# Performance work log

Hardware: AMD Instinct MI355X
Metric: run time of the kernel (lower is better)

The kernel has to match this reference:

```python
import jax, jax.numpy as jnp
import numpy as np

N_NODES = 50000
N_EDGES = 800000
IN_CH, HIDDEN, OUT_CH = 128, 128, 64
EPS = 1e-5


def setup_inputs() -> dict:
    key = jax.random.key(0)
    ks = jax.random.split(key, 16)
    s = lambda fan_in: 1.0 / np.sqrt(fan_in)
    return {
        "x": jax.random.normal(ks[0], (N_NODES, IN_CH), dtype=jnp.float32),
        "edge_index": jax.random.randint(ks[1], (2, N_EDGES), 0, N_NODES, dtype=jnp.int64),
        # SAGEConv1: lin_l (neighbors, with bias), lin_r (root, no bias)
        "Wl1": jax.random.uniform(ks[2], (HIDDEN, IN_CH), jnp.float32, -s(IN_CH), s(IN_CH)),
        "bl1": jnp.zeros((HIDDEN,), jnp.float32),
        "Wr1": jax.random.uniform(ks[3], (HIDDEN, IN_CH), jnp.float32, -s(IN_CH), s(IN_CH)),
        # SAGEConv2
        "Wl2": jax.random.uniform(ks[4], (HIDDEN, HIDDEN), jnp.float32, -s(HIDDEN), s(HIDDEN)),
        "bl2": jnp.zeros((HIDDEN,), jnp.float32),
        "Wr2": jax.random.uniform(ks[5], (HIDDEN, HIDDEN), jnp.float32, -s(HIDDEN), s(HIDDEN)),
        # SAGEConv3
        "Wl3": jax.random.uniform(ks[6], (OUT_CH, HIDDEN), jnp.float32, -s(HIDDEN), s(HIDDEN)),
        "bl3": jnp.zeros((OUT_CH,), jnp.float32),
        "Wr3": jax.random.uniform(ks[7], (OUT_CH, HIDDEN), jnp.float32, -s(HIDDEN), s(HIDDEN)),
        # LayerNorms
        "g1": jnp.ones((HIDDEN,), jnp.float32),
        "beta1": jnp.zeros((HIDDEN,), jnp.float32),
        "g2": jnp.ones((HIDDEN,), jnp.float32),
        "beta2": jnp.zeros((HIDDEN,), jnp.float32),
    }


def _sage_conv(x, src, dst, n_nodes, Wl, bl, Wr):
    # mean aggregation of source features at target nodes (PyG SAGEConv, aggr='mean')
    msg = x[src]                                             # [E, C] gather
    sums = jax.ops.segment_sum(msg, dst, num_segments=n_nodes)
    cnt = jax.ops.segment_sum(jnp.ones((src.shape[0],), x.dtype), dst, num_segments=n_nodes)
    mean = sums / jnp.maximum(cnt, 1.0)[:, None]
    return mean @ Wl.T + bl + x @ Wr.T


def _layernorm(h, g, b):
    mu = jnp.mean(h, axis=-1, keepdims=True)
    var = jnp.mean(jnp.square(h - mu), axis=-1, keepdims=True)
    return (h - mu) * jax.lax.rsqrt(var + EPS) * g + b


def reference(x, edge_index, Wl1, bl1, Wr1, Wl2, bl2, Wr2, Wl3, bl3, Wr3, g1, beta1, g2, beta2):
    src, dst = edge_index[0], edge_index[1]
    n = x.shape[0]
    h = jax.nn.relu(_sage_conv(x, src, dst, n, Wl1, bl1, Wr1))
    h = _layernorm(h, g1, beta1)
    h = jax.nn.relu(_sage_conv(h, src, dst, n, Wl2, bl2, Wr2))
    h = _layernorm(h, g2, beta2)
    return _sage_conv(h, src, dst, n, Wl3, bl3, Wr3)
```

## Files before the change

kernel.cpp:

```cpp
#include <hip/hip_runtime.h>

#define NNODES 50000
#define NEDGES 800000
#define FILL_CHUNK 7168
#define FILL_NCHUNK 112
#define FILL_BLOCKS (FILL_NCHUNK * 8)
#define GEMM_BLOCKS ((NNODES + 127) / 128)
#define CAP 64

using bf16x8  = __attribute__((ext_vector_type(8))) __bf16;
using floatx4 = __attribute__((ext_vector_type(4))) float;

__device__ __forceinline__ float bf2f(unsigned short u) {
  unsigned int v = ((unsigned int)u) << 16;
  return __builtin_bit_cast(float, v);
}
__device__ __forceinline__ unsigned short f2bf(float f) {
  unsigned int u = __builtin_bit_cast(unsigned int, f);
  u += 0x7fffu + ((u >> 16) & 1u);
  return (unsigned short)(u >> 16);
}

__device__ __forceinline__ signed char enc_i8(float f) {
  float g = fminf(fmaxf(f * 32.0f, -127.0f), 127.0f);
  return (signed char)__float2int_rn(g);
}

struct WPtrs {
  const float* src[6];
  unsigned short* dst[6];
  int n[6];
};

__global__ __launch_bounds__(256) void convw_zero_kernel(WPtrs p, int* __restrict__ cnt) {
  if (blockIdx.x < 320) {
    int i = blockIdx.x * 256 + threadIdx.x;
#pragma unroll
    for (int s = 0; s < 6; ++s) {
      if (i < p.n[s]) {
        p.dst[s][i] = f2bf(p.src[s][i]);
        return;
      }
      i -= p.n[s];
    }
  } else {
    int i = (blockIdx.x - 320) * 256 + threadIdx.x;
    if (i < NNODES) cnt[i] = 0;
  }
}

__device__ __forceinline__ void fill_body(int bid, const int* __restrict__ src,
                                          const int* __restrict__ dst,
                                          int* __restrict__ cnt,
                                          int* __restrict__ bucket) {
  int p = bid & 7;
  if (p == 7) return;
  int chunk = bid >> 3;
  int e0 = chunk * FILL_CHUNK;
  int e1 = min(e0 + FILL_CHUNK, NEDGES);
  for (int base = e0 + (int)threadIdx.x * 4; base < e1; base += 256 * 4) {
    int4 d4 = *(const int4*)(dst + base);
    int4 s4 = *(const int4*)(src + base);
    if ((d4.x >> 13) == p) { int sl = atomicAdd(&cnt[d4.x], 1); if (sl < CAP) bucket[(size_t)d4.x * CAP + sl] = s4.x; }
    if ((d4.y >> 13) == p) { int sl = atomicAdd(&cnt[d4.y], 1); if (sl < CAP) bucket[(size_t)d4.y * CAP + sl] = s4.y; }
    if ((d4.z >> 13) == p) { int sl = atomicAdd(&cnt[d4.z], 1); if (sl < CAP) bucket[(size_t)d4.z * CAP + sl] = s4.z; }
    if ((d4.w >> 13) == p) { int sl = atomicAdd(&cnt[d4.w], 1); if (sl < CAP) bucket[(size_t)d4.w * CAP + sl] = s4.w; }
  }
}

__device__ __forceinline__ bf16x8 load_frag(const unsigned short* p) {
  uint4 v = *(const uint4*)p;
  return __builtin_bit_cast(bf16x8, v);
}
__device__ __forceinline__ bf16x8 cvt_frag(const float* p) {
  float4 v0 = *(const float4*)p;
  float4 v1 = *(const float4*)(p + 4);
  uint4 o;
  o.x = (unsigned int)f2bf(v0.x) | ((unsigned int)f2bf(v0.y) << 16);
  o.y = (unsigned int)f2bf(v0.z) | ((unsigned int)f2bf(v0.w) << 16);
  o.z = (unsigned int)f2bf(v1.x) | ((unsigned int)f2bf(v1.y) << 16);
  o.w = (unsigned int)f2bf(v1.z) | ((unsigned int)f2bf(v1.w) << 16);
  return __builtin_bit_cast(bf16x8, o);
}

template <int NTL, int NTR, bool F32IN>
__device__ __forceinline__ void gemm_dual_body(int bid, const void* __restrict__ Ain,
                                               const unsigned short* __restrict__ W,
                                               signed char* __restrict__ yl,
                                               unsigned short* __restrict__ yr) {
  constexpr int NT = NTL + NTR;
  int wave = threadIdx.x >> 6;
  int lane = threadIdx.x & 63;
  int quad = lane >> 4;
  int m = lane & 15;
  int row0 = bid * 128 + wave * 32;
  int ar0 = min(row0 + m, NNODES - 1);
  int ar1 = min(row0 + 16 + m, NNODES - 1);
  bf16x8 a0[4], a1[4];
#pragma unroll
  for (int kt = 0; kt < 4; ++kt) {
    if constexpr (F32IN) {
      const float* A = (const float*)Ain;
      a0[kt] = cvt_frag(A + (size_t)ar0 * 128 + quad * 8 + kt * 32);
      a1[kt] = cvt_frag(A + (size_t)ar1 * 128 + quad * 8 + kt * 32);
    } else {
      const unsigned short* A = (const unsigned short*)Ain;
      a0[kt] = load_frag(A + (size_t)ar0 * 128 + quad * 8 + kt * 32);
      a1[kt] = load_frag(A + (size_t)ar1 * 128 + quad * 8 + kt * 32);
    }
  }
#pragma unroll
  for (int t = 0; t < NT; ++t) {
    const unsigned short* wp = W + (t * 16 + m) * 128 + quad * 8;
    bf16x8 w[4];
#pragma unroll
    for (int kt = 0; kt < 4; ++kt) w[kt] = load_frag(wp + kt * 32);
    floatx4 c0 = {0.f, 0.f, 0.f, 0.f};
    floatx4 c1 = {0.f, 0.f, 0.f, 0.f};
#pragma unroll
    for (int kt = 0; kt < 4; ++kt) {
      c0 = __builtin_amdgcn_mfma_f32_16x16x32_bf16(a0[kt], w[kt], c0, 0, 0, 0);
      c1 = __builtin_amdgcn_mfma_f32_16x16x32_bf16(a1[kt], w[kt], c1, 0, 0, 0);
    }
#pragma unroll
    for (int r = 0; r < 4; ++r) {
      int g0 = row0 + quad * 4 + r;
      int g1r = g0 + 16;
      if (t < NTL) {
        int col = t * 16 + m;
        if (g0 < NNODES) yl[(size_t)g0 * (NTL * 16) + col] = enc_i8(c0[r]);
        if (g1r < NNODES) yl[(size_t)g1r * (NTL * 16) + col] = enc_i8(c1[r]);
      } else {
        int col = (t - NTL) * 16 + m;
        if (g0 < NNODES) yr[(size_t)g0 * (NTR * 16) + col] = f2bf(c0[r]);
        if (g1r < NNODES) yr[(size_t)g1r * (NTR * 16) + col] = f2bf(c1[r]);
      }
    }
  }
}

__global__ __launch_bounds__(256) void fill_gemm1_kernel(
    const int* __restrict__ src, const int* __restrict__ dst, int* __restrict__ cnt,
    int* __restrict__ bucket, const float* __restrict__ x,
    const unsigned short* __restrict__ W, signed char* __restrict__ yl,
    unsigned short* __restrict__ yr) {
  if (blockIdx.x < FILL_BLOCKS)
    fill_body(blockIdx.x, src, dst, cnt, bucket);
  else
    gemm_dual_body<8, 8, true>(blockIdx.x - FILL_BLOCKS, x, W, yl, yr);
}

template <int NTL, int NTR, bool F32IN>
__global__ __launch_bounds__(256) void gemm_dual_kernel(
    const void* __restrict__ Ain, const unsigned short* __restrict__ W,
    signed char* __restrict__ yl, unsigned short* __restrict__ yr) {
  gemm_dual_body<NTL, NTR, F32IN>(blockIdx.x, Ain, W, yl, yr);
}

#define ACCU(u, base)                                       \
  a[base] += (int)((signed char)((u) & 0xffu));             \
  a[base + 1] += (int)((signed char)(((u) >> 8) & 0xffu));  \
  a[base + 2] += (int)((signed char)(((u) >> 16) & 0xffu)); \
  a[base + 3] += (int)((signed char)((u) >> 24));
#define ACC16(v) ACCU((v).x, 0) ACCU((v).y, 4) ACCU((v).z, 8) ACCU((v).w, 12)

__global__ __launch_bounds__(256) void agg_ln_kernel(
    const signed char* __restrict__ yl, const unsigned short* __restrict__ yr,
    const float* __restrict__ bl, const float* __restrict__ g,
    const float* __restrict__ be, const int* __restrict__ cnt,
    const int* __restrict__ bucket, unsigned short* __restrict__ hout) {
  int wid = (blockIdx.x * blockDim.x + threadIdx.x) >> 6;
  int lane = threadIdx.x & 63;
  int grp = lane >> 3;
  int c8 = lane & 7;
  int gw = wid * 8 + grp;
  if (gw >= NNODES) return;
  int offc = c8 * 16;
  int deg = cnt[gw];
  int ed = min(deg, CAP);
  const int* bk = bucket + (size_t)gw * CAP;
  int a[16];
#pragma unroll
  for (int k = 0; k < 16; ++k) a[k] = 0;
  int e = 0;
  for (; e + 3 < ed; e += 4) {
    int i0 = bk[e], i1 = bk[e + 1], i2 = bk[e + 2], i3 = bk[e + 3];
    uint4 v0 = *(const uint4*)(yl + (size_t)i0 * 128 + offc);
    uint4 v1 = *(const uint4*)(yl + (size_t)i1 * 128 + offc);
    uint4 v2 = *(const uint4*)(yl + (size_t)i2 * 128 + offc);
    uint4 v3 = *(const uint4*)(yl + (size_t)i3 * 128 + offc);
    ACC16(v0) ACC16(v1) ACC16(v2) ACC16(v3)
  }
  if (e + 1 < ed) {
    int i0 = bk[e], i1 = bk[e + 1];
    uint4 v0 = *(const uint4*)(yl + (size_t)i0 * 128 + offc);
    uint4 v1 = *(const uint4*)(yl + (size_t)i1 * 128 + offc);
    ACC16(v0) ACC16(v1)
    e += 2;
  }
  if (e < ed) {
    int i0 = bk[e];
    uint4 v = *(const uint4*)(yl + (size_t)i0 * 128 + offc);
    ACC16(v)
  }
  float idg = 0.03125f / (float)((deg > 0) ? deg : 1);
  const unsigned short* yrp = yr + (size_t)gw * 128 + offc;
  uint4 r0 = *(const uint4*)yrp;
  uint4 r1 = *(const uint4*)(yrp + 8);
  unsigned rw[8] = {r0.x, r0.y, r0.z, r0.w, r1.x, r1.y, r1.z, r1.w};
  float blv[16], gv[16], bev[16];
#pragma unroll
  for (int k = 0; k < 4; ++k) {
    *(float4*)&blv[k * 4] = *(const float4*)(bl + offc + k * 4);
    *(float4*)&gv[k * 4] = *(const float4*)(g + offc + k * 4);
    *(float4*)&bev[k * 4] = *(const float4*)(be + offc + k * 4);
  }
  float x[16], sA = 0.f, sB = 0.f;
#pragma unroll
  for (int k = 0; k < 16; ++k) {
    float rv = bf2f((unsigned short)((rw[k >> 1] >> ((k & 1) * 16)) & 0xffffu));
    float xv = (float)a[k] * idg + rv + blv[k];
    xv = fmaxf(xv, 0.f);
    x[k] = xv;
    sA += xv;
    sB += xv * xv;
  }
#pragma unroll
  for (int msk = 1; msk < 8; msk <<= 1) {
    sA += __shfl_xor(sA, msk, 8);
    sB += __shfl_xor(sB, msk, 8);
  }
  float mu = sA * (1.0f / 128.0f);
  float var = sB * (1.0f / 128.0f) - mu * mu;
  float rs = rsqrtf(var + 1e-5f);
  unsigned ow[8];
#pragma unroll
  for (int k = 0; k < 8; ++k) {
    float y0 = (x[2 * k] - mu) * rs * gv[2 * k] + bev[2 * k];
    float y1 = (x[2 * k + 1] - mu) * rs * gv[2 * k + 1] + bev[2 * k + 1];
    ow[k] = (unsigned)f2bf(y0) | ((unsigned)f2bf(y1) << 16);
  }
  uint4* op = (uint4*)(hout + (size_t)gw * 128 + offc);
  op[0] = make_uint4(ow[0], ow[1], ow[2], ow[3]);
  op[1] = make_uint4(ow[4], ow[5], ow[6], ow[7]);
}

__global__ __launch_bounds__(256) void agg3_kernel(
    const signed char* __restrict__ yl, const unsigned short* __restrict__ yr,
    const float* __restrict__ bl, const int* __restrict__ cnt,
    const int* __restrict__ bucket, float* __restrict__ out) {
  int wid = (blockIdx.x * blockDim.x + threadIdx.x) >> 6;
  int lane = threadIdx.x & 63;
  int grp = lane >> 2;
  int c4 = lane & 3;
  int gw = wid * 16 + grp;
  if (gw >= NNODES) return;
  int offc = c4 * 16;
  int deg = cnt[gw];
  int ed = min(deg, CAP);
  const int* bk = bucket + (size_t)gw * CAP;
  int a[16];
#pragma unroll
  for (int k = 0; k < 16; ++k) a[k] = 0;
  int e = 0;
  for (; e + 3 < ed; e += 4) {
    int i0 = bk[e], i1 = bk[e + 1], i2 = bk[e + 2], i3 = bk[e + 3];
    uint4 v0 = *(const uint4*)(yl + (size_t)i0 * 64 + offc);
    uint4 v1 = *(const uint4*)(yl + (size_t)i1 * 64 + offc);
    uint4 v2 = *(const uint4*)(yl + (size_t)i2 * 64 + offc);
    uint4 v3 = *(const uint4*)(yl + (size_t)i3 * 64 + offc);
    ACC16(v0) ACC16(v1) ACC16(v2) ACC16(v3)
  }
  if (e + 1 < ed) {
    int i0 = bk[e], i1 = bk[e + 1];
    uint4 v0 = *(const uint4*)(yl + (size_t)i0 * 64 + offc);
    uint4 v1 = *(const uint4*)(yl + (size_t)i1 * 64 + offc);
    ACC16(v0) ACC16(v1)
    e += 2;
  }
  if (e < ed) {
    int i0 = bk[e];
    uint4 v = *(const uint4*)(yl + (size_t)i0 * 64 + offc);
    ACC16(v)
  }
  float idg = 0.03125f / (float)((deg > 0) ? deg : 1);
  const unsigned short* yrp = yr + (size_t)gw * 64 + offc;
  uint4 r0 = *(const uint4*)yrp;
  uint4 r1 = *(const uint4*)(yrp + 8);
  unsigned rw[8] = {r0.x, r0.y, r0.z, r0.w, r1.x, r1.y, r1.z, r1.w};
  float blv[16];
#pragma unroll
  for (int k = 0; k < 4; ++k)
    *(float4*)&blv[k * 4] = *(const float4*)(bl + offc + k * 4);
  float o[16];
#pragma unroll
  for (int k = 0; k < 16; ++k) {
    float rv = bf2f((unsigned short)((rw[k >> 1] >> ((k & 1) * 16)) & 0xffffu));
    o[k] = (float)a[k] * idg + rv + blv[k];
  }
  float* op = out + (size_t)gw * 64 + offc;
#pragma unroll
  for (int k = 0; k < 4; ++k) *(float4*)(op + k * 4) = *(float4*)&o[k * 4];
}

extern "C" void kernel_launch(void* const* d_in, const int* in_sizes, int n_in,
                              void* d_out, int out_size, void* d_ws, size_t ws_size,
                              hipStream_t stream) {
  const float* x = (const float*)d_in[0];
  const int* ei = (const int*)d_in[1];
  const int* srcv = ei;
  const int* dstv = ei + NEDGES;
  const float* Wl1 = (const float*)d_in[2];
  const float* bl1 = (const float*)d_in[3];
  const float* Wr1 = (const float*)d_in[4];
  const float* Wl2 = (const float*)d_in[5];
  const float* bl2 = (const float*)d_in[6];
  const float* Wr2 = (const float*)d_in[7];
  const float* Wl3 = (const float*)d_in[8];
  const float* bl3 = (const float*)d_in[9];
  const float* Wr3 = (const float*)d_in[10];
  const float* g1 = (const float*)d_in[11];
  const float* be1 = (const float*)d_in[12];
  const float* g2 = (const float*)d_in[13];
  const float* be2 = (const float*)d_in[14];

  char* ws = (char*)d_ws;
  size_t o = 0;
  int* cnt = (int*)(ws + o);      o += 200192;
  int* bucket = (int*)(ws + o);   o += (size_t)NNODES * CAP * 4;
  unsigned short* wb1 = (unsigned short*)(ws + o); o += 65536;
  unsigned short* wb2 = (unsigned short*)(ws + o); o += 65536;
  unsigned short* wb3 = (unsigned short*)(ws + o); o += 32768;
  signed char* yl1 = (signed char*)(ws + o);       o += (size_t)50000 * 128;
  unsigned short* yr1 = (unsigned short*)(ws + o); o += (size_t)50000 * 256;
  unsigned short* h1 = (unsigned short*)(ws + o);  o += (size_t)50000 * 256;
  signed char* yl2 = (signed char*)(ws + o);       o += (size_t)50000 * 128;
  unsigned short* yr2 = (unsigned short*)(ws + o); o += (size_t)50000 * 256;
  unsigned short* h2 = (unsigned short*)(ws + o);  o += (size_t)50000 * 256;
  signed char* yl3 = (signed char*)(ws + o);       o += (size_t)50000 * 64;
  unsigned short* yr3 = (unsigned short*)(ws + o); o += (size_t)50000 * 128;

  dim3 blk(256);
  dim3 aggGrid((NNODES + 31) / 32);
  dim3 agg3Grid((NNODES + 63) / 64);
  dim3 gemmGrid(GEMM_BLOCKS);

  WPtrs wp;
  wp.src[0] = Wl1; wp.dst[0] = wb1;         wp.n[0] = 128 * 128;
  wp.src[1] = Wr1; wp.dst[1] = wb1 + 16384; wp.n[1] = 128 * 128;
  wp.src[2] = Wl2; wp.dst[2] = wb2;         wp.n[2] = 128 * 128;
  wp.src[3] = Wr2; wp.dst[3] = wb2 + 16384; wp.n[3] = 128 * 128;
  wp.src[4] = Wl3; wp.dst[4] = wb3;         wp.n[4] = 64 * 128;
  wp.src[5] = Wr3; wp.dst[5] = wb3 + 8192;  wp.n[5] = 64 * 128;

  convw_zero_kernel<<<dim3(320 + 196), blk, 0, stream>>>(wp, cnt);
  fill_gemm1_kernel<<<dim3(FILL_BLOCKS + GEMM_BLOCKS), blk, 0, stream>>>(
      srcv, dstv, cnt, bucket, x, wb1, yl1, yr1);
  agg_ln_kernel<<<aggGrid, blk, 0, stream>>>(yl1, yr1, bl1, g1, be1, cnt, bucket, h1);
  gemm_dual_kernel<8, 8, false><<<gemmGrid, blk, 0, stream>>>(h1, wb2, yl2, yr2);
  agg_ln_kernel<<<aggGrid, blk, 0, stream>>>(yl2, yr2, bl2, g2, be2, cnt, bucket, h2);
  gemm_dual_kernel<4, 4, false><<<gemmGrid, blk, 0, stream>>>(h2, wb3, yl3, yr3);
  agg3_kernel<<<agg3Grid, blk, 0, stream>>>(yl3, yr3, bl3, cnt, bucket, (float*)d_out);
}
```

Baseline: 242.5 us.

## Queue fill edges in LDS and pad degree counters to avoid atomic contention

The bucket-fill phase now compacts matching edges into a shared-memory queue with wave ballots, then issues global atomics and nontemporal bucket stores in a separate batched phase. Degree counters are strided (32 or 4 ints apart, depending on workspace size) so that atomics to neighbouring nodes land on different cache lines. Edge loads are also made nontemporal. The aim is to cut atomic contention and memory-latency stalls in the fill, at the cost of a larger counter array to zero, strided counter reads in the aggregation kernels, and a queue capped at QCAP entries that could drop edges if a block's partition overflows it.

```diff
diff --git a/kernel.cpp b/kernel.cpp
--- a/kernel.cpp
+++ b/kernel.cpp
@@ -7,9 +7,11 @@
 #define FILL_BLOCKS (FILL_NCHUNK * 8)
 #define GEMM_BLOCKS ((NNODES + 127) / 128)
 #define CAP 64
+#define QCAP 2048
 
 using bf16x8  = __attribute__((ext_vector_type(8))) __bf16;
 using floatx4 = __attribute__((ext_vector_type(4))) float;
+using intx4   = __attribute__((ext_vector_type(4))) int;
 
 __device__ __forceinline__ float bf2f(unsigned short u) {
   unsigned int v = ((unsigned int)u) << 16;
@@ -32,7 +34,8 @@
   int n[6];
 };
 
-__global__ __launch_bounds__(256) void convw_zero_kernel(WPtrs p, int* __restrict__ cnt) {
+__global__ __launch_bounds__(256) void convw_zero_kernel(WPtrs p, int* __restrict__ cnt,
+                                                         int tot4) {
   if (blockIdx.x < 320) {
     int i = blockIdx.x * 256 + threadIdx.x;
 #pragma unroll
@@ -45,26 +48,69 @@
     }
   } else {
     int i = (blockIdx.x - 320) * 256 + threadIdx.x;
-    if (i < NNODES) cnt[i] = 0;
+    int4* q = (int4*)cnt;
+    int j0 = i * 2, j1 = i * 2 + 1;
+    int4 z = make_int4(0, 0, 0, 0);
+    if (j0 < tot4) q[j0] = z;
+    if (j1 < tot4) q[j1] = z;
   }
 }
 
 __device__ __forceinline__ void fill_body(int bid, const int* __restrict__ src,
                                           const int* __restrict__ dst,
                                           int* __restrict__ cnt,
-                                          int* __restrict__ bucket) {
+                                          int* __restrict__ bucket, int cs) {
   int p = bid & 7;
   if (p == 7) return;
+  __shared__ int qd[QCAP];
+  __shared__ int qs[QCAP];
+  __shared__ int qn;
+  if (threadIdx.x == 0) qn = 0;
+  __syncthreads();
+  int lane = threadIdx.x & 63;
   int chunk = bid >> 3;
   int e0 = chunk * FILL_CHUNK;
   int e1 = min(e0 + FILL_CHUNK, NEDGES);
   for (int base = e0 + (int)threadIdx.x * 4; base < e1; base += 256 * 4) {
-    int4 d4 = *(const int4*)(dst + base);
-    int4 s4 = *(const int4*)(src + base);
-    if ((d4.x >> 13) == p) { int sl = atomicAdd(&cnt[d4.x], 1); if (sl < CAP) bucket[(size_t)d4.x * CAP + sl] = s4.x; }
-    if ((d4.y >> 13) == p) { int sl = atomicAdd(&cnt[d4.y], 1); if (sl < CAP) bucket[(size_t)d4.y * CAP + sl] = s4.y; }
-    if ((d4.z >> 13) == p) { int sl = atomicAdd(&cnt[d4.z], 1); if (sl < CAP) bucket[(size_t)d4.z * CAP + sl] = s4.z; }
-    if ((d4.w >> 13) == p) { int sl = atomicAdd(&cnt[d4.w], 1); if (sl < CAP) bucket[(size_t)d4.w * CAP + sl] = s4.w; }
+    intx4 d4 = __builtin_nontemporal_load((const intx4*)(dst + base));
+    intx4 s4 = __builtin_nontemporal_load((const intx4*)(src + base));
+    int dv[4] = {d4[0], d4[1], d4[2], d4[3]};
+    int sv[4] = {s4[0], s4[1], s4[2], s4[3]};
+#pragma unroll
+    for (int k = 0; k < 4; ++k) {
+      bool mk = (dv[k] >> 13) == p;
+      unsigned long long mask = __ballot(mk);
+      if (mask) {
+        int ldr = __builtin_ctzll(mask);
+        int basq = 0;
+        if (lane == ldr) basq = atomicAdd(&qn, (int)__popcll(mask));
+        basq = __shfl(basq, ldr);
+        if (mk) {
+          int t = basq + (int)__popcll(mask & ((1ull << lane) - 1ull));
+          if (t < QCAP) { qd[t] = dv[k]; qs[t] = sv[k]; }
+        }
+      }
+    }
+  }
+  __syncthreads();
+  int n = qn;
+  if (n > QCAP) n = QCAP;
+  int dd[8], ss[8], sl[8];
+#pragma unroll
+  for (int j = 0; j < 8; ++j) {
+    int i = (int)threadIdx.x + j * 256;
+    if (i < n) { dd[j] = qd[i]; ss[j] = qs[i]; }
+  }
+#pragma unroll
+  for (int j = 0; j < 8; ++j) {
+    int i = (int)threadIdx.x + j * 256;
+    if (i < n) sl[j] = atomicAdd(&cnt[(size_t)dd[j] * cs], 1);
+  }
+#pragma unroll
+  for (int j = 0; j < 8; ++j) {
+    int i = (int)threadIdx.x + j * 256;
+    if (i < n && sl[j] < CAP)
+      __builtin_nontemporal_store(ss[j], &bucket[(size_t)dd[j] * CAP + sl[j]]);
   }
 }
 
@@ -143,9 +189,9 @@
     const int* __restrict__ src, const int* __restrict__ dst, int* __restrict__ cnt,
     int* __restrict__ bucket, const float* __restrict__ x,
     const unsigned short* __restrict__ W, signed char* __restrict__ yl,
-    unsigned short* __restrict__ yr) {
+    unsigned short* __restrict__ yr, int cs) {
   if (blockIdx.x < FILL_BLOCKS)
-    fill_body(blockIdx.x, src, dst, cnt, bucket);
+    fill_body(blockIdx.x, src, dst, cnt, bucket, cs);
   else
     gemm_dual_body<8, 8, true>(blockIdx.x - FILL_BLOCKS, x, W, yl, yr);
 }
@@ -168,7 +214,7 @@
     const signed char* __restrict__ yl, const unsigned short* __restrict__ yr,
     const float* __restrict__ bl, const float* __restrict__ g,
     const float* __restrict__ be, const int* __restrict__ cnt,
-    const int* __restrict__ bucket, unsigned short* __restrict__ hout) {
+    const int* __restrict__ bucket, unsigned short* __restrict__ hout, int cs) {
   int wid = (blockIdx.x * blockDim.x + threadIdx.x) >> 6;
   int lane = threadIdx.x & 63;
   int grp = lane >> 3;
@@ -176,7 +222,7 @@
   int gw = wid * 8 + grp;
   if (gw >= NNODES) return;
   int offc = c8 * 16;
-  int deg = cnt[gw];
+  int deg = cnt[(size_t)gw * cs];
   int ed = min(deg, CAP);
   const int* bk = bucket + (size_t)gw * CAP;
   int a[16];
@@ -248,7 +294,7 @@
 __global__ __launch_bounds__(256) void agg3_kernel(
     const signed char* __restrict__ yl, const unsigned short* __restrict__ yr,
     const float* __restrict__ bl, const int* __restrict__ cnt,
-    const int* __restrict__ bucket, float* __restrict__ out) {
+    const int* __restrict__ bucket, float* __restrict__ out, int cs) {
   int wid = (blockIdx.x * blockDim.x + threadIdx.x) >> 6;
   int lane = threadIdx.x & 63;
   int grp = lane >> 2;
@@ -256,7 +302,7 @@
   int gw = wid * 16 + grp;
   if (gw >= NNODES) return;
   int offc = c4 * 16;
-  int deg = cnt[gw];
+  int deg = cnt[(size_t)gw * cs];
   int ed = min(deg, CAP);
   const int* bk = bucket + (size_t)gw * CAP;
   int a[16];
@@ -324,9 +370,12 @@
   const float* g2 = (const float*)d_in[13];
   const float* be2 = (const float*)d_in[14];
 
+  int cs = (ws_size >= (size_t)94000000) ? 32 : 4;
+
   char* ws = (char*)d_ws;
   size_t o = 0;
-  int* cnt = (int*)(ws + o);      o += 200192;
+  int* cnt = (int*)(ws + o);
+  o += (((size_t)NNODES * cs * 4) + 255) & ~(size_t)255;
   int* bucket = (int*)(ws + o);   o += (size_t)NNODES * CAP * 4;
   unsigned short* wb1 = (unsigned short*)(ws + o); o += 65536;
   unsigned short* wb2 = (unsigned short*)(ws + o); o += 65536;
@@ -353,12 +402,14 @@
   wp.src[4] = Wl3; wp.dst[4] = wb3;         wp.n[4] = 64 * 128;
   wp.src[5] = Wr3; wp.dst[5] = wb3 + 8192;  wp.n[5] = 64 * 128;
 
-  convw_zero_kernel<<<dim3(320 + 196), blk, 0, stream>>>(wp, cnt);
+  int tot4 = NNODES * cs / 4;
+  int zblocks = (tot4 + 511) / 512;
+  convw_zero_kernel<<<dim3(320 + zblocks), blk, 0, stream>>>(wp, cnt, tot4);
   fill_gemm1_kernel<<<dim3(FILL_BLOCKS + GEMM_BLOCKS), blk, 0, stream>>>(
-      srcv, dstv, cnt, bucket, x, wb1, yl1, yr1);
-  agg_ln_kernel<<<aggGrid, blk, 0, stream>>>(yl1, yr1, bl1, g1, be1, cnt, bucket, h1);
+      srcv, dstv, cnt, bucket, x, wb1, yl1, yr1, cs);
+  agg_ln_kernel<<<aggGrid, blk, 0, stream>>>(yl1, yr1, bl1, g1, be1, cnt, bucket, h1, cs);
   gemm_dual_kernel<8, 8, false><<<gemmGrid, blk, 0, stream>>>(h1, wb2, yl2, yr2);
-  agg_ln_kernel<<<aggGrid, blk, 0, stream>>>(yl2, yr2, bl2, g2, be2, cnt, bucket, h2);
+  agg_ln_kernel<<<aggGrid, blk, 0, stream>>>(yl2, yr2, bl2, g2, be2, cnt, bucket, h2, cs);
   gemm_dual_kernel<4, 4, false><<<gemmGrid, blk, 0, stream>>>(h2, wb3, yl3, yr3);
-  agg3_kernel<<<agg3Grid, blk, 0, stream>>>(yl3, yr3, bl3, cnt, bucket, (float*)d_out);
-}
+  agg3_kernel<<<agg3Grid, blk, 0, stream>>>(yl3, yr3, bl3, cnt, bucket, (float*)d_out, cs);
+}
```

After: 264.4 us. 9.0% more time.

## Fuse aggregation+LayerNorm with following dual GEMM through shared memory

Applied to the files above, without the earlier changes.

Merges the agg_ln kernel and the next layer's dual GEMM into one 1024-thread kernel. Each block aggregates and normalizes 128 nodes, stages the bf16 result in padded LDS, then 8 waves run MFMA against the weights and write the int8 and bf16 outputs. This removes the h1/h2 round trips through global memory and two kernel launches. In exchange, 1024-thread blocks with a large LDS tile may lower occupancy, half the waves sit idle during the GEMM phase, and output stores are scalar per element.

```diff
diff --git a/kernel.cpp b/kernel.cpp
--- a/kernel.cpp
+++ b/kernel.cpp
@@ -6,7 +6,9 @@
 #define FILL_NCHUNK 112
 #define FILL_BLOCKS (FILL_NCHUNK * 8)
 #define GEMM_BLOCKS ((NNODES + 127) / 128)
+#define FUSE_BLOCKS ((NNODES + 127) / 128)
 #define CAP 64
+#define HSTRIDE 136
 
 using bf16x8  = __attribute__((ext_vector_type(8))) __bf16;
 using floatx4 = __attribute__((ext_vector_type(4))) float;
@@ -150,13 +152,6 @@
     gemm_dual_body<8, 8, true>(blockIdx.x - FILL_BLOCKS, x, W, yl, yr);
 }
 
-template <int NTL, int NTR, bool F32IN>
-__global__ __launch_bounds__(256) void gemm_dual_kernel(
-    const void* __restrict__ Ain, const unsigned short* __restrict__ W,
-    signed char* __restrict__ yl, unsigned short* __restrict__ yr) {
-  gemm_dual_body<NTL, NTR, F32IN>(blockIdx.x, Ain, W, yl, yr);
-}
-
 #define ACCU(u, base)                                       \
   a[base] += (int)((signed char)((u) & 0xffu));             \
   a[base + 1] += (int)((signed char)(((u) >> 8) & 0xffu));  \
@@ -164,57 +159,57 @@
   a[base + 3] += (int)((signed char)((u) >> 24));
 #define ACC16(v) ACCU((v).x, 0) ACCU((v).y, 4) ACCU((v).z, 8) ACCU((v).w, 12)
 
-__global__ __launch_bounds__(256) void agg_ln_kernel(
-    const signed char* __restrict__ yl, const unsigned short* __restrict__ yr,
+template <int NTL, int NTR>
+__global__ __launch_bounds__(1024) void aggln_gemm_kernel(
+    const signed char* __restrict__ yl_in, const unsigned short* __restrict__ yr_in,
     const float* __restrict__ bl, const float* __restrict__ g,
     const float* __restrict__ be, const int* __restrict__ cnt,
-    const int* __restrict__ bucket, unsigned short* __restrict__ hout) {
-  int wid = (blockIdx.x * blockDim.x + threadIdx.x) >> 6;
-  int lane = threadIdx.x & 63;
-  int grp = lane >> 3;
-  int c8 = lane & 7;
-  int gw = wid * 8 + grp;
-  if (gw >= NNODES) return;
+    const int* __restrict__ bucket, const unsigned short* __restrict__ W,
+    signed char* __restrict__ yl_out, unsigned short* __restrict__ yr_out) {
+  constexpr int NT = NTL + NTR;
+  __shared__ unsigned short hlds[128 * HSTRIDE];
+  int tid = (int)threadIdx.x;
+  int lg = tid >> 3;
+  int c8 = tid & 7;
+  int gw = blockIdx.x * 128 + lg;
+  int gwc = min(gw, NNODES - 1);
   int offc = c8 * 16;
-  int deg = cnt[gw];
+  int deg = cnt[gwc];
   int ed = min(deg, CAP);
-  const int* bk = bucket + (size_t)gw * CAP;
+  const int* bk = bucket + (size_t)gwc * CAP;
   int a[16];
 #pragma unroll
   for (int k = 0; k < 16; ++k) a[k] = 0;
   int e = 0;
   for (; e + 3 < ed; e += 4) {
     int i0 = bk[e], i1 = bk[e + 1], i2 = bk[e + 2], i3 = bk[e + 3];
-    uint4 v0 = *(const uint4*)(yl + (size_t)i0 * 128 + offc);
-    uint4 v1 = *(const uint4*)(yl + (size_t)i1 * 128 + offc);
-    uint4 v2 = *(const uint4*)(yl + (size_t)i2 * 128 + offc);
-    uint4 v3 = *(const uint4*)(yl + (size_t)i3 * 128 + offc);
+    uint4 v0 = *(const uint4*)(yl_in + (size_t)i0 * 128 + offc);
+    uint4 v1 = *(const uint4*)(yl_in + (size_t)i1 * 128 + offc);
+    uint4 v2 = *(const uint4*)(yl_in + (size_t)i2 * 128 + offc);
+    uint4 v3 = *(const uint4*)(yl_in + (size_t)i3 * 128 + offc);
     ACC16(v0) ACC16(v1) ACC16(v2) ACC16(v3)
   }
   if (e + 1 < ed) {
     int i0 = bk[e], i1 = bk[e + 1];
-    uint4 v0 = *(const uint4*)(yl + (size_t)i0 * 128 + offc);
-    uint4 v1 = *(const uint4*)(yl + (size_t)i1 * 128 + offc);
+    uint4 v0 = *(const uint4*)(yl_in + (size_t)i0 * 128 + offc);
+    uint4 v1 = *(const uint4*)(yl_in + (size_t)i1 * 128 + offc);
     ACC16(v0) ACC16(v1)
     e += 2;
   }
   if (e < ed) {
     int i0 = bk[e];
-    uint4 v = *(const uint4*)(yl + (size_t)i0 * 128 + offc);
+    uint4 v = *(const uint4*)(yl_in + (size_t)i0 * 128 + offc);
     ACC16(v)
   }
   float idg = 0.03125f / (float)((deg > 0) ? deg : 1);
-  const unsigned short* yrp = yr + (size_t)gw * 128 + offc;
+  const unsigned short* yrp = yr_in + (size_t)gwc * 128 + offc;
   uint4 r0 = *(const uint4*)yrp;
   uint4 r1 = *(const uint4*)(yrp + 8);
   unsigned rw[8] = {r0.x, r0.y, r0.z, r0.w, r1.x, r1.y, r1.z, r1.w};
-  float blv[16], gv[16], bev[16];
-#pragma unroll
-  for (int k = 0; k < 4; ++k) {
+  float blv[16];
+#pragma unroll
+  for (int k = 0; k < 4; ++k)
     *(float4*)&blv[k * 4] = *(const float4*)(bl + offc + k * 4);
-    *(float4*)&gv[k * 4] = *(const float4*)(g + offc + k * 4);
-    *(float4*)&bev[k * 4] = *(const float4*)(be + offc + k * 4);
-  }
   float x[16], sA = 0.f, sB = 0.f;
 #pragma unroll
   for (int k = 0; k < 16; ++k) {
@@ -233,6 +228,12 @@
   float mu = sA * (1.0f / 128.0f);
   float var = sB * (1.0f / 128.0f) - mu * mu;
   float rs = rsqrtf(var + 1e-5f);
+  float gv[16], bev[16];
+#pragma unroll
+  for (int k = 0; k < 4; ++k) {
+    *(float4*)&gv[k * 4] = *(const float4*)(g + offc + k * 4);
+    *(float4*)&bev[k * 4] = *(const float4*)(be + offc + k * 4);
+  }
   unsigned ow[8];
 #pragma unroll
   for (int k = 0; k < 8; ++k) {
@@ -240,9 +241,42 @@
     float y1 = (x[2 * k + 1] - mu) * rs * gv[2 * k + 1] + bev[2 * k + 1];
     ow[k] = (unsigned)f2bf(y0) | ((unsigned)f2bf(y1) << 16);
   }
-  uint4* op = (uint4*)(hout + (size_t)gw * 128 + offc);
-  op[0] = make_uint4(ow[0], ow[1], ow[2], ow[3]);
-  op[1] = make_uint4(ow[4], ow[5], ow[6], ow[7]);
+  uint4* hp = (uint4*)&hlds[lg * HSTRIDE + offc];
+  hp[0] = make_uint4(ow[0], ow[1], ow[2], ow[3]);
+  hp[1] = make_uint4(ow[4], ow[5], ow[6], ow[7]);
+  __syncthreads();
+  int wave = tid >> 6;
+  if (wave >= 8) return;
+  int lane = tid & 63;
+  int quad = lane >> 4;
+  int m = lane & 15;
+  int row0 = blockIdx.x * 128 + wave * 16;
+  int lr = wave * 16 + m;
+  bf16x8 a0[4];
+#pragma unroll
+  for (int kt = 0; kt < 4; ++kt)
+    a0[kt] = load_frag(&hlds[lr * HSTRIDE + quad * 8 + kt * 32]);
+#pragma unroll
+  for (int t = 0; t < NT; ++t) {
+    const unsigned short* wp = W + (t * 16 + m) * 128 + quad * 8;
+    bf16x8 w[4];
+#pragma unroll
+    for (int kt = 0; kt < 4; ++kt) w[kt] = load_frag(wp + kt * 32);
+    floatx4 c0 = {0.f, 0.f, 0.f, 0.f};
+#pragma unroll
+    for (int kt = 0; kt < 4; ++kt)
+      c0 = __builtin_amdgcn_mfma_f32_16x16x32_bf16(a0[kt], w[kt], c0, 0, 0, 0);
+#pragma unroll
+    for (int r = 0; r < 4; ++r) {
+      int g0 = row0 + quad * 4 + r;
+      if (g0 < NNODES) {
+        if (t < NTL)
+          yl_out[(size_t)g0 * (NTL * 16) + t * 16 + m] = enc_i8(c0[r]);
+        else
+          yr_out[(size_t)g0 * (NTR * 16) + (t - NTL) * 16 + m] = f2bf(c0[r]);
+      }
+    }
+  }
 }
 
 __global__ __launch_bounds__(256) void agg3_kernel(
@@ -333,17 +367,14 @@
   unsigned short* wb3 = (unsigned short*)(ws + o); o += 32768;
   signed char* yl1 = (signed char*)(ws + o);       o += (size_t)50000 * 128;
   unsigned short* yr1 = (unsigned short*)(ws + o); o += (size_t)50000 * 256;
-  unsigned short* h1 = (unsigned short*)(ws + o);  o += (size_t)50000 * 256;
   signed char* yl2 = (signed char*)(ws + o);       o += (size_t)50000 * 128;
   unsigned short* yr2 = (unsigned short*)(ws + o); o += (size_t)50000 * 256;
-  unsigned short* h2 = (unsigned short*)(ws + o);  o += (size_t)50000 * 256;
   signed char* yl3 = (signed char*)(ws + o);       o += (size_t)50000 * 64;
   unsigned short* yr3 = (unsigned short*)(ws + o); o += (size_t)50000 * 128;
 
   dim3 blk(256);
-  dim3 aggGrid((NNODES + 31) / 32);
+  dim3 fblk(1024);
   dim3 agg3Grid((NNODES + 63) / 64);
-  dim3 gemmGrid(GEMM_BLOCKS);
 
   WPtrs wp;
   wp.src[0] = Wl1; wp.dst[0] = wb1;         wp.n[0] = 128 * 128;
@@ -356,9 +387,9 @@
   convw_zero_kernel<<<dim3(320 + 196), blk, 0, stream>>>(wp, cnt);
   fill_gemm1_kernel<<<dim3(FILL_BLOCKS + GEMM_BLOCKS), blk, 0, stream>>>(
       srcv, dstv, cnt, bucket, x, wb1, yl1, yr1);
-  agg_ln_kernel<<<aggGrid, blk, 0, stream>>>(yl1, yr1, bl1, g1, be1, cnt, bucket, h1);
-  gemm_dual_kernel<8, 8, false><<<gemmGrid, blk, 0, stream>>>(h1, wb2, yl2, yr2);
-  agg_ln_kernel<<<aggGrid, blk, 0, stream>>>(yl2, yr2, bl2, g2, be2, cnt, bucket, h2);
-  gemm_dual_kernel<4, 4, false><<<gemmGrid, blk, 0, stream>>>(h2, wb3, yl3, yr3);
+  aggln_gemm_kernel<8, 8><<<dim3(FUSE_BLOCKS), fblk, 0, stream>>>(
+      yl1, yr1, bl1, g1, be1, cnt, bucket, wb2, yl2, yr2);
+  aggln_gemm_kernel<4, 4><<<dim3(FUSE_BLOCKS), fblk, 0, stream>>>(
+      yl2, yr2, bl2, g2, be2, cnt, bucket, wb3, yl3, yr3);
   agg3_kernel<<<agg3Grid, blk, 0, stream>>>(yl3, yr3, bl3, cnt, bucket, (float*)d_out);
 }
```

After: 264.6 us. 1.09x slower.
